# Performance work log

Measured on AMD Instinct MI355X. Metric: run time of the kernel, lower is better.

The kernel has to match this reference:

```python
import jax, jax.numpy as jnp
import numpy as np

Q_DIM = 512
K_DIM = 512
V_DIM = 512
H_DIM = 256
B, Q, K = 4, 512, 512


def setup_inputs() -> dict:
    key = jax.random.key(0)
    ks = jax.random.split(key, 7)
    q = jax.random.normal(ks[0], (B, Q, Q_DIM), dtype=jnp.float32)
    k = jax.random.normal(ks[1], (B, K, K_DIM), dtype=jnp.float32)
    v = jax.random.normal(ks[2], (B, K, V_DIM), dtype=jnp.float32)
    S = jax.random.randint(ks[3], (B,), 1, K + 1, dtype=jnp.int64)
    # learned params (nn.Linear stores weight of shape (out, in); y = x @ W.T)
    Wq = jax.random.normal(ks[4], (H_DIM, Q_DIM), dtype=jnp.float32) / np.sqrt(Q_DIM)
    Wk = jax.random.normal(ks[5], (H_DIM, K_DIM), dtype=jnp.float32) / np.sqrt(K_DIM)
    w = jax.random.normal(ks[6], (H_DIM,), dtype=jnp.float32) / np.sqrt(H_DIM)
    return {"q": q, "k": k, "v": v, "S": S, "Wq": Wq, "Wk": Wk, "w": w}


def reference(q, k, v, S, Wq, Wk, w):
    # Additive (Bahdanau) attention scores.
    pq = jnp.einsum('bqd,hd->bqh', q, Wq)            # (B, Q, H)
    pk = jnp.einsum('bkd,hd->bkh', k, Wk)            # (B, K, H)
    t = jnp.tanh(pq[:, :, None, :] + pk[:, None, :, :])  # (B, Q, K, H)
    scores = jnp.einsum('bqkh,h->bqk', t, w)         # (B, Q, K)
    # mask keys with index >= S[b] to -inf
    kv_idx = jnp.arange(scores.shape[-1])            # (K,)
    mask = kv_idx[None, None, :] >= S[:, None, None] # (B, 1, K) -> broadcast
    scores = jnp.where(mask, -jnp.inf, scores)
    return scores
```

## Files before the change

### kernel.cpp

```cpp
#include <hip/hip_runtime.h>
#include <hip/hip_bf16.h>
#include <math.h>

#define QDIM 512
#define HDIM 256
#define QQ 512
#define KKE 512

#define TWO_LOG2E 2.8853900817779268f
#define MASK_VAL -1.0e30f

typedef __attribute__((ext_vector_type(8))) short bf16x8;
typedef __attribute__((ext_vector_type(4))) float f32x4;

__device__ __forceinline__ unsigned int pk2(float x, float y) {
  __hip_bfloat162 h = __float22bfloat162_rn(make_float2(x, y));
  unsigned int u;
  __builtin_memcpy(&u, &h, 4);
  return u;
}

__global__ __launch_bounds__(512) void proj_kernel(
    const float* __restrict__ qin, const float* __restrict__ kin,
    const float* __restrict__ Wq, const float* __restrict__ Wk,
    const float* __restrict__ wvec,
    float* __restrict__ EqT, unsigned short* __restrict__ EkT,
    float* __restrict__ wsum_out) {
  __shared__ __align__(16) unsigned short As[32 * 72];
  __shared__ __align__(16) unsigned short Bs[64 * 72];

  const int tid = threadIdx.x;
  const int lane = tid & 63;
  const int wv = __builtin_amdgcn_readfirstlane(tid >> 6);
  const int quad = lane >> 4;
  const int l16 = lane & 15;

  const int m0 = blockIdx.x * 32;
  const int h0 = blockIdx.y * 64;
  const bool isk = (blockIdx.z != 0);
  const float* A = isk ? kin : qin;
  const float* W = isk ? Wk : Wq;

  const int srow = tid >> 4;
  const int sg = (tid & 15) * 4;

  const float* arow_g = &A[(size_t)(m0 + srow) * QDIM + sg];
  const float* brow0_g = &W[(size_t)(h0 + srow) * QDIM + sg];
  const float* brow1_g = &W[(size_t)(h0 + srow + 32) * QDIM + sg];
  unsigned short* adst = &As[srow * 72 + sg];
  unsigned short* bdst0 = &Bs[srow * 72 + sg];
  unsigned short* bdst1 = &Bs[(srow + 32) * 72 + sg];

  const unsigned short* afrag = &As[((wv & 1) * 16 + l16) * 72 + quad * 8];
  const unsigned short* bfrag = &Bs[((wv >> 1) * 16 + l16) * 72 + quad * 8];

  f32x4 acc = (f32x4){0.f, 0.f, 0.f, 0.f};

  float4 pa = *(const float4*)arow_g;
  float4 pb0 = *(const float4*)brow0_g;
  float4 pb1 = *(const float4*)brow1_g;

  for (int kc = 0; kc < QDIM; kc += 64) {
    __syncthreads();
    *(uint2*)adst = make_uint2(pk2(pa.x, pa.y), pk2(pa.z, pa.w));
    *(uint2*)bdst0 = make_uint2(pk2(pb0.x, pb0.y), pk2(pb0.z, pb0.w));
    *(uint2*)bdst1 = make_uint2(pk2(pb1.x, pb1.y), pk2(pb1.z, pb1.w));
    if (kc + 64 < QDIM) {
      pa = *(const float4*)(arow_g + kc + 64);
      pb0 = *(const float4*)(brow0_g + kc + 64);
      pb1 = *(const float4*)(brow1_g + kc + 64);
    }
    __syncthreads();
    bf16x8 a0 = *(const bf16x8*)afrag;
    bf16x8 a1 = *(const bf16x8*)(afrag + 32);
    bf16x8 b0 = *(const bf16x8*)bfrag;
    bf16x8 b1 = *(const bf16x8*)(bfrag + 32);
    acc = __builtin_amdgcn_mfma_f32_16x16x32_bf16(a0, b0, acc, 0, 0, 0);
    acc = __builtin_amdgcn_mfma_f32_16x16x32_bf16(a1, b1, acc, 0, 0, 0);
  }

  const int b = m0 >> 9;
  const int hrow = h0 + (wv >> 1) * 16 + l16;
  const int mcol = (m0 & 511) + (wv & 1) * 16 + quad * 4;
  float e0 = __builtin_amdgcn_exp2f(acc[0] * TWO_LOG2E);
  float e1 = __builtin_amdgcn_exp2f(acc[1] * TWO_LOG2E);
  float e2 = __builtin_amdgcn_exp2f(acc[2] * TWO_LOG2E);
  float e3 = __builtin_amdgcn_exp2f(acc[3] * TWO_LOG2E);
  if (!isk) {
    *(float4*)(EqT + ((size_t)b * HDIM + hrow) * 512 + mcol) =
        make_float4(e0, e1, e2, e3);
    if (m0 == 0 && h0 == 0 && tid < 64) {
      float s = wvec[tid] + wvec[tid + 64] + wvec[tid + 128] + wvec[tid + 192];
#pragma unroll
      for (int off = 32; off; off >>= 1) s += __shfl_down(s, off);
      if (tid == 0) wsum_out[0] = s;
    }
  } else {
    *(uint2*)(EkT + ((size_t)b * HDIM + hrow) * 512 + mcol) =
        make_uint2(pk2(e0, e1), pk2(e2, e3));
  }
}

__global__ __launch_bounds__(256) void score_kernel(
    const float* __restrict__ EqT, const unsigned short* __restrict__ EkT,
    const float* __restrict__ wvec, const float* __restrict__ wsump,
    const int* __restrict__ Sraw, float* __restrict__ out) {
  const int b = blockIdx.z;
  const int q0 = blockIdx.y * 16;
  const int i = blockIdx.x;
  const int S = (Sraw[1] == 0) ? Sraw[2 * b] : Sraw[b];
  const int tid = threadIdx.x;
  const int wv = __builtin_amdgcn_readfirstlane(tid >> 6);
  const int L = tid & 63;
  const int q = L >> 2;
  const int k8 = (L & 3) * 8;

  __shared__ float wl[HDIM];
  __shared__ float Eqs[256][16];
  __shared__ float Eks[256][32];
  __shared__ float Cmb[4][64][8];

  const int T[4] = {i, 7 - i, 8 + i, 15 - i};
  bool lv[4];
#pragma unroll
  for (int j = 0; j < 4; j++) lv[j] = (T[j] * 32) < S;

  const int mq = 4 * wv + (L >> 2);
  const int mkg = (L & 3) * 8;
  float* obase = out + ((size_t)(b * QQ + q0 + mq) * KKE) + mkg;
  const float4 m4 = make_float4(MASK_VAL, MASK_VAL, MASK_VAL, MASK_VAL);

  if (lv[0]) {
    const float wsum = wsump[0];
    const float* EqB = EqT + (size_t)b * (HDIM * QQ) + q0;
    const unsigned short* EkB = EkT + (size_t)b * (HDIM * KKE);
    const int hr = tid >> 2;
    const int cq = (tid & 3) * 4;
    const int ce = (tid & 3) * 8;

    wl[tid] = wvec[tid];
    uint4 kr[4];
#pragma unroll
    for (int p = 0; p < 4; p++) {
      *(float4*)&Eqs[hr + p * 64][cq] =
          *(const float4*)&EqB[(size_t)(hr + p * 64) * QQ + cq];
      kr[p] = *(const uint4*)(EkB + (size_t)(hr + p * 64) * KKE + T[0] * 32 + ce);
    }
#pragma unroll
    for (int p = 0; p < 4; p++) {
      uint4 u = kr[p];
      *(float4*)&Eks[hr + p * 64][ce] = make_float4(
          __uint_as_float(u.x << 16), __uint_as_float(u.x & 0xffff0000u),
          __uint_as_float(u.y << 16), __uint_as_float(u.y & 0xffff0000u));
      *(float4*)&Eks[hr + p * 64][ce + 4] = make_float4(
          __uint_as_float(u.z << 16), __uint_as_float(u.z & 0xffff0000u),
          __uint_as_float(u.w << 16), __uint_as_float(u.w & 0xffff0000u));
    }
    __syncthreads();

    const int hbase = wv * 64;
    auto tile_pass = [&]() {
      float a0 = 0.f, a1 = 0.f, a2 = 0.f, a3 = 0.f;
      float a4 = 0.f, a5 = 0.f, a6 = 0.f, a7 = 0.f;
#pragma unroll 4
      for (int hh = 0; hh < 64; hh++) {
        const int h = hbase + hh;
        float wh = wl[h];
        float eq = Eqs[h][q];
        float4 u0 = *(const float4*)&Eks[h][k8];
        float4 u1 = *(const float4*)&Eks[h][k8 + 4];
        a0 = fmaf(wh, __builtin_amdgcn_rcpf(fmaf(eq, u0.x, 1.f)), a0);
        a1 = fmaf(wh, __builtin_amdgcn_rcpf(fmaf(eq, u0.y, 1.f)), a1);
        a2 = fmaf(wh, __builtin_amdgcn_rcpf(fmaf(eq, u0.z, 1.f)), a2);
        a3 = fmaf(wh, __builtin_amdgcn_rcpf(fmaf(eq, u0.w, 1.f)), a3);
        a4 = fmaf(wh, __builtin_amdgcn_rcpf(fmaf(eq, u1.x, 1.f)), a4);
        a5 = fmaf(wh, __builtin_amdgcn_rcpf(fmaf(eq, u1.y, 1.f)), a5);
        a6 = fmaf(wh, __builtin_amdgcn_rcpf(fmaf(eq, u1.z, 1.f)), a6);
        a7 = fmaf(wh, __builtin_amdgcn_rcpf(fmaf(eq, u1.w, 1.f)), a7);
      }
      *(float4*)&Cmb[wv][L][0] = make_float4(a0, a1, a2, a3);
      *(float4*)&Cmb[wv][L][4] = make_float4(a4, a5, a6, a7);
    };

    auto sum_store = [&](int kbase) {
      if (L < 16) {
        const int Ls = 16 * wv + L;
        float s0 = 0.f, s1 = 0.f, s2 = 0.f, s3 = 0.f;
        float s4 = 0.f, s5 = 0.f, s6 = 0.f, s7 = 0.f;
#pragma unroll
        for (int w = 0; w < 4; w++) {
          float4 c0 = *(const float4*)&Cmb[w][Ls][0];
          float4 c1 = *(const float4*)&Cmb[w][Ls][4];
          s0 += c0.x; s1 += c0.y; s2 += c0.z; s3 += c0.w;
          s4 += c1.x; s5 += c1.y; s6 += c1.z; s7 += c1.w;
        }
        const int kb = kbase + mkg;
        float4 r0, r1;
        r0.x = (kb + 0 < S) ? (wsum - 2.f * s0) : MASK_VAL;
        r0.y = (kb + 1 < S) ? (wsum - 2.f * s1) : MASK_VAL;
        r0.z = (kb + 2 < S) ? (wsum - 2.f * s2) : MASK_VAL;
        r0.w = (kb + 3 < S) ? (wsum - 2.f * s3) : MASK_VAL;
        r1.x = (kb + 4 < S) ? (wsum - 2.f * s4) : MASK_VAL;
        r1.y = (kb + 5 < S) ? (wsum - 2.f * s5) : MASK_VAL;
        r1.z = (kb + 6 < S) ? (wsum - 2.f * s6) : MASK_VAL;
        r1.w = (kb + 7 < S) ? (wsum - 2.f * s7) : MASK_VAL;
        float* mrow = obase + kbase;
        *(float4*)&mrow[0] = r0;
        *(float4*)&mrow[4] = r1;
      }
    };

#pragma unroll 1
    for (int j = 0; j < 4; j++) {
      if (!lv[j]) break;
      const bool pn = (j + 1 < 4) && lv[j + 1];
      if (pn) {
#pragma unroll
        for (int p = 0; p < 4; p++)
          kr[p] = *(const uint4*)(EkB + (size_t)(hr + p * 64) * KKE +
                                  T[j + 1] * 32 + ce);
      }
      tile_pass();
      __syncthreads();
      if (pn) {
#pragma unroll
        for (int p = 0; p < 4; p++) {
          uint4 u = kr[p];
          *(float4*)&Eks[hr + p * 64][ce] = make_float4(
              __uint_as_float(u.x << 16), __uint_as_float(u.x & 0xffff0000u),
              __uint_as_float(u.y << 16), __uint_as_float(u.y & 0xffff0000u));
          *(float4*)&Eks[hr + p * 64][ce + 4] = make_float4(
              __uint_as_float(u.z << 16), __uint_as_float(u.z & 0xffff0000u),
              __uint_as_float(u.w << 16), __uint_as_float(u.w & 0xffff0000u));
        }
      }
      sum_store(T[j] * 32);
      if (pn) __syncthreads();
    }
  }

#pragma unroll
  for (int j = 0; j < 4; j++) {
    if (!lv[j] && L < 16) {
      float* mrow = obase + T[j] * 32;
      *(float4*)&mrow[0] = m4;
      *(float4*)&mrow[4] = m4;
    }
  }
}

extern "C" void kernel_launch(void* const* d_in, const int* in_sizes, int n_in,
                              void* d_out, int out_size, void* d_ws, size_t ws_size,
                              hipStream_t stream) {
  const float* q  = (const float*)d_in[0];
  const float* k  = (const float*)d_in[1];
  const int*   S  = (const int*)d_in[3];
  const float* Wq = (const float*)d_in[4];
  const float* Wk = (const float*)d_in[5];
  const float* w  = (const float*)d_in[6];
  float* out = (float*)d_out;

  float* wsf = (float*)d_ws;
  float* EqT = wsf;
  unsigned short* EkT = (unsigned short*)(wsf + 524288);
  float* wsum = wsf + 524288 + 262144;

  proj_kernel<<<dim3(64, 4, 2), 512, 0, stream>>>(q, k, Wq, Wk, w, EqT, EkT, wsum);
  score_kernel<<<dim3(4, 32, 4), 256, 0, stream>>>(EqT, EkT, w, wsum, S, out);
}
```

Measured before the change: 99.82 us.

## Pair hidden units to share one reciprocal per two terms

The score loop adds pairs of hidden units as one fraction, w1/A + w2/B = (w1*B + w2*A)/(A*B). This halves the rcp transcendental instructions and uses packed two-wide FMAs. To support this, Eq, Ek and w are restaged in shared memory with adjacent hidden units interleaved, with padded row strides. The cost is extra multiplies and adds, scalar (non-vector) shared stores during staging, and a risk that the A*B product overflows for large exponentials, which could give inf/NaN.

```diff
diff --git a/kernel.cpp b/kernel.cpp
--- a/kernel.cpp
+++ b/kernel.cpp
@@ -12,6 +12,7 @@
 
 typedef __attribute__((ext_vector_type(8))) short bf16x8;
 typedef __attribute__((ext_vector_type(4))) float f32x4;
+typedef __attribute__((ext_vector_type(2))) float f32x2;
 
 __device__ __forceinline__ unsigned int pk2(float x, float y) {
   __hip_bfloat162 h = __float22bfloat162_rn(make_float2(x, y));
@@ -115,10 +116,10 @@
   const int q = L >> 2;
   const int k8 = (L & 3) * 8;
 
-  __shared__ float wl[HDIM];
-  __shared__ float Eqs[256][16];
-  __shared__ float Eks[256][32];
-  __shared__ float Cmb[4][64][8];
+  __shared__ __align__(16) float ws2a[128][2];
+  __shared__ __align__(16) float Eqs2[128][34];
+  __shared__ __align__(16) float Eks2[128][68];
+  __shared__ __align__(16) float Cmb[4][64][8];
 
   const int T[4] = {i, 7 - i, 8 + i, 15 - i};
   bool lv[4];
@@ -138,45 +139,72 @@
     const int cq = (tid & 3) * 4;
     const int ce = (tid & 3) * 8;
 
-    wl[tid] = wvec[tid];
+    if (tid < 128) {
+      float2 g = *(const float2*)&wvec[2 * tid];
+      ws2a[tid][0] = g.y;
+      ws2a[tid][1] = g.x;
+    }
     uint4 kr[4];
 #pragma unroll
     for (int p = 0; p < 4; p++) {
-      *(float4*)&Eqs[hr + p * 64][cq] =
-          *(const float4*)&EqB[(size_t)(hr + p * 64) * QQ + cq];
-      kr[p] = *(const uint4*)(EkB + (size_t)(hr + p * 64) * KKE + T[0] * 32 + ce);
+      const int h = hr + p * 64;
+      float4 g = *(const float4*)&EqB[(size_t)h * QQ + cq];
+      float* d = &Eqs2[h >> 1][h & 1];
+      d[(cq + 0) * 2] = g.x;
+      d[(cq + 1) * 2] = g.y;
+      d[(cq + 2) * 2] = g.z;
+      d[(cq + 3) * 2] = g.w;
+      kr[p] = *(const uint4*)(EkB + (size_t)h * KKE + T[0] * 32 + ce);
     }
 #pragma unroll
     for (int p = 0; p < 4; p++) {
+      const int h = hr + p * 64;
+      float* d = &Eks2[h >> 1][h & 1];
       uint4 u = kr[p];
-      *(float4*)&Eks[hr + p * 64][ce] = make_float4(
-          __uint_as_float(u.x << 16), __uint_as_float(u.x & 0xffff0000u),
-          __uint_as_float(u.y << 16), __uint_as_float(u.y & 0xffff0000u));
-      *(float4*)&Eks[hr + p * 64][ce + 4] = make_float4(
-          __uint_as_float(u.z << 16), __uint_as_float(u.z & 0xffff0000u),
-          __uint_as_float(u.w << 16), __uint_as_float(u.w & 0xffff0000u));
+      d[(ce + 0) * 2] = __uint_as_float(u.x << 16);
+      d[(ce + 1) * 2] = __uint_as_float(u.x & 0xffff0000u);
+      d[(ce + 2) * 2] = __uint_as_float(u.y << 16);
+      d[(ce + 3) * 2] = __uint_as_float(u.y & 0xffff0000u);
+      d[(ce + 4) * 2] = __uint_as_float(u.z << 16);
+      d[(ce + 5) * 2] = __uint_as_float(u.z & 0xffff0000u);
+      d[(ce + 6) * 2] = __uint_as_float(u.w << 16);
+      d[(ce + 7) * 2] = __uint_as_float(u.w & 0xffff0000u);
     }
     __syncthreads();
 
-    const int hbase = wv * 64;
+    const int pbase = wv * 32;
     auto tile_pass = [&]() {
       float a0 = 0.f, a1 = 0.f, a2 = 0.f, a3 = 0.f;
       float a4 = 0.f, a5 = 0.f, a6 = 0.f, a7 = 0.f;
+      const f32x2 one2 = (f32x2){1.f, 1.f};
 #pragma unroll 4
-      for (int hh = 0; hh < 64; hh++) {
-        const int h = hbase + hh;
-        float wh = wl[h];
-        float eq = Eqs[h][q];
-        float4 u0 = *(const float4*)&Eks[h][k8];
-        float4 u1 = *(const float4*)&Eks[h][k8 + 4];
-        a0 = fmaf(wh, __builtin_amdgcn_rcpf(fmaf(eq, u0.x, 1.f)), a0);
-        a1 = fmaf(wh, __builtin_amdgcn_rcpf(fmaf(eq, u0.y, 1.f)), a1);
-        a2 = fmaf(wh, __builtin_amdgcn_rcpf(fmaf(eq, u0.z, 1.f)), a2);
-        a3 = fmaf(wh, __builtin_amdgcn_rcpf(fmaf(eq, u0.w, 1.f)), a3);
-        a4 = fmaf(wh, __builtin_amdgcn_rcpf(fmaf(eq, u1.x, 1.f)), a4);
-        a5 = fmaf(wh, __builtin_amdgcn_rcpf(fmaf(eq, u1.y, 1.f)), a5);
-        a6 = fmaf(wh, __builtin_amdgcn_rcpf(fmaf(eq, u1.z, 1.f)), a6);
-        a7 = fmaf(wh, __builtin_amdgcn_rcpf(fmaf(eq, u1.w, 1.f)), a7);
+      for (int pp = 0; pp < 32; pp++) {
+        const int p = pbase + pp;
+        const f32x2 ws = *(const f32x2*)&ws2a[p][0];
+        const f32x2 eq = *(const f32x2*)&Eqs2[p][q * 2];
+        const float* er = &Eks2[p][k8 * 2];
+        float4 u0 = *(const float4*)(er);
+        float4 u1 = *(const float4*)(er + 4);
+        float4 u2 = *(const float4*)(er + 8);
+        float4 u3 = *(const float4*)(er + 12);
+#define PAIR_TERM(ex, ey, acc)                                         \
+        {                                                              \
+          f32x2 AB = __builtin_elementwise_fma(eq, (f32x2){ex, ey},    \
+                                               one2);                  \
+          f32x2 m = ws * AB;                                           \
+          float N = m.x + m.y;                                         \
+          float D = AB.x * AB.y;                                       \
+          acc = fmaf(N, __builtin_amdgcn_rcpf(D), acc);                \
+        }
+        PAIR_TERM(u0.x, u0.y, a0)
+        PAIR_TERM(u0.z, u0.w, a1)
+        PAIR_TERM(u1.x, u1.y, a2)
+        PAIR_TERM(u1.z, u1.w, a3)
+        PAIR_TERM(u2.x, u2.y, a4)
+        PAIR_TERM(u2.z, u2.w, a5)
+        PAIR_TERM(u3.x, u3.y, a6)
+        PAIR_TERM(u3.z, u3.w, a7)
+#undef PAIR_TERM
       }
       *(float4*)&Cmb[wv][L][0] = make_float4(a0, a1, a2, a3);
       *(float4*)&Cmb[wv][L][4] = make_float4(a4, a5, a6, a7);
@@ -225,13 +253,17 @@
       if (pn) {
 #pragma unroll
         for (int p = 0; p < 4; p++) {
+          const int h = hr + p * 64;
+          float* d = &Eks2[h >> 1][h & 1];
           uint4 u = kr[p];
-          *(float4*)&Eks[hr + p * 64][ce] = make_float4(
-              __uint_as_float(u.x << 16), __uint_as_float(u.x & 0xffff0000u),
-              __uint_as_float(u.y << 16), __uint_as_float(u.y & 0xffff0000u));
-          *(float4*)&Eks[hr + p * 64][ce + 4] = make_float4(
-              __uint_as_float(u.z << 16), __uint_as_float(u.z & 0xffff0000u),
-              __uint_as_float(u.w << 16), __uint_as_float(u.w & 0xffff0000u));
+          d[(ce + 0) * 2] = __uint_as_float(u.x << 16);
+          d[(ce + 1) * 2] = __uint_as_float(u.x & 0xffff0000u);
+          d[(ce + 2) * 2] = __uint_as_float(u.y << 16);
+          d[(ce + 3) * 2] = __uint_as_float(u.y & 0xffff0000u);
+          d[(ce + 4) * 2] = __uint_as_float(u.z << 16);
+          d[(ce + 5) * 2] = __uint_as_float(u.z & 0xffff0000u);
+          d[(ce + 6) * 2] = __uint_as_float(u.w << 16);
+          d[(ce + 7) * 2] = __uint_as_float(u.w & 0xffff0000u);
         }
       }
       sum_store(T[j] * 32);
```

After: 101.8 us. About the same (+1.9%).
